# Kernel tuning notes

Measured on AMD Instinct MI355X. Metric: run time of the kernel, lower is better.

The kernel has to match this reference:

```python
import jax, jax.numpy as jnp
import numpy as np

N_NODES = 8192
EMBED = 64
HID = [256, 256, 128]
ACTION = 8192


def setup_inputs() -> dict:
    key = jax.random.key(0)
    ks = jax.random.split(key, 16)
    state = jax.random.uniform(ks[0], (N_NODES, N_NODES), dtype=jnp.float32)
    start = 100  # python int node index
    def u(k, shape, fan_out):
        s = 1.0 / np.sqrt(fan_out)
        return jax.random.uniform(k, shape, minval=-s, maxval=s, dtype=jnp.float32)
    def xav(k, shape):
        s = np.sqrt(6.0 / (shape[0] + shape[1]))
        return jax.random.uniform(k, shape, minval=-s, maxval=s, dtype=jnp.float32)
    in_size = N_NODES + EMBED
    return {
        "state": state,
        "start": start,
        "gc1_w": u(ks[1], (1, HID[0]), HID[0]),
        "gc1_b": u(ks[2], (HID[0],), HID[0]),
        "gc2_w": u(ks[3], (HID[0], EMBED), EMBED),
        "gc2_b": u(ks[4], (EMBED,), EMBED),
        "fc1_w": xav(ks[5], (HID[0], in_size)),
        "fc1_b": jnp.zeros((HID[0],), jnp.float32),
        "fc2_w": xav(ks[6], (HID[1], HID[0])),
        "fc2_b": jnp.zeros((HID[1],), jnp.float32),
        "fc3_w": xav(ks[7], (HID[2], HID[1])),
        "fc3_b": jnp.zeros((HID[2],), jnp.float32),
        "fc4_w": xav(ks[8], (ACTION, HID[2])),
        "fc4_b": jnp.zeros((ACTION,), jnp.float32),
    }


def reference(state, start, gc1_w, gc1_b, gc2_w, gc2_b,
              fc1_w, fc1_b, fc2_w, fc2_b, fc3_w, fc3_b, fc4_w, fc4_b):
    n = state.shape[0]
    # node features = diagonal of state, shape [N, 1]
    x = jnp.diagonal(state)[:, None]
    # adjacency: state with zeroed diagonal, detached (no grad to state via adj)
    idx = jnp.arange(n)
    adj = jax.lax.stop_gradient(state.at[idx, idx].set(0.0))
    # GCN layer 1: spmm(adj, x @ W) + b, relu  (dropout inactive: eval mode)
    h = jax.nn.relu(adj @ (x @ gc1_w) + gc1_b)          # [N, 256]
    # GCN layer 2
    h = jax.nn.relu(adj @ (h @ gc2_w) + gc2_b)          # [N, 64]
    h = jax.nn.log_softmax(h, axis=1)
    start_embedding = h[start]                           # [64]
    start_features = state[start, :]                     # [N]
    e = jnp.concatenate([start_features, start_embedding], axis=-1)  # [N+64]
    y = jax.nn.relu(e @ fc1_w.T + fc1_b)
    y = jax.nn.relu(y @ fc2_w.T + fc2_b)
    y = jax.nn.relu(y @ fc3_w.T + fc3_b)
    end_q = jax.nn.relu(y @ fc4_w.T + fc4_b)             # [action_size]
    return end_q
```

## Files before the change

### kernel.cpp

```cpp
#include <hip/hip_runtime.h>

#define NODES 8192
#define H1 256
#define EMB 64
#define IN_SIZE (NODES + EMB)
#define HID3 128
#define NPART 256

#define X_OFF    0
#define S_OFF    (X_OFF + NODES)
#define PART_OFF (S_OFF + NODES)
#define LS_OFF   (PART_OFF + NPART*H1)
#define Y1_OFF   (LS_OFF + EMB)
#define Y3_OFF   (Y1_OFF + H1)

__device__ __forceinline__ float waveReduceSum(float v) {
    #pragma unroll
    for (int off = 32; off > 0; off >>= 1) v += __shfl_down(v, off, 64);
    return v;
}

__global__ __launch_bounds__(256) void k_diag(const float* __restrict__ state,
                                              float* __restrict__ x) {
    int i = blockIdx.x * 256 + threadIdx.x;
    x[i] = state[(size_t)i * NODES + i];
}

__global__ __launch_bounds__(256) void k_row(const float* __restrict__ state,
                                             const float* __restrict__ x,
                                             float* __restrict__ s) {
    __shared__ float red[4];
    const int i = blockIdx.x;
    const int tid = threadIdx.x;
    const float4* row4 = (const float4*)(state + (size_t)i * NODES);
    const float4* x4   = (const float4*)x;

    float acc = 0.f;
    #pragma unroll
    for (int it = 0; it < NODES / 4 / 256; ++it) {
        int j = tid + it * 256;
        float4 r = row4[j];
        float4 xv = x4[j];
        acc += r.x * xv.x + r.y * xv.y + r.z * xv.z + r.w * xv.w;
    }
    acc = waveReduceSum(acc);
    if ((tid & 63) == 0) red[tid >> 6] = acc;
    __syncthreads();
    if (tid == 0) {
        float xi = x[i];
        s[i] = red[0] + red[1] + red[2] + red[3] - xi * xi;
    }
}

__global__ __launch_bounds__(256) void k_tpart(const float* __restrict__ s,
                                               const float* __restrict__ state,
                                               const int* __restrict__ pstart,
                                               const float* __restrict__ w1,
                                               const float* __restrict__ b1,
                                               float* __restrict__ part) {
    __shared__ float ls_s[32], ls_a[32];
    const int b = blockIdx.x, t = threadIdx.x;
    const int start = *pstart;
    if (t < 32) {
        int i = b * 32 + t;
        ls_s[t] = s[i];
        float a = state[(size_t)start * NODES + i];
        ls_a[t] = (i == start) ? 0.f : a;
    }
    __syncthreads();
    const float w = w1[t], bb = b1[t];
    float acc = 0.f;
    #pragma unroll
    for (int q = 0; q < 32; ++q)
        acc += ls_a[q] * fmaxf(ls_s[q] * w + bb, 0.f);
    part[b * H1 + t] = acc;
}

__global__ __launch_bounds__(256) void k_sm(const float* __restrict__ part,
                                            const float* __restrict__ w2,
                                            const float* __restrict__ b2,
                                            float* __restrict__ ls) {
    __shared__ float ts[H1];
    const int t = threadIdx.x;
    float acc = 0.f;
    #pragma unroll 8
    for (int b = 0; b < NPART; ++b) acc += part[b * H1 + t];
    ts[t] = acc;
    __syncthreads();
    if (t < EMB) {
        float u = 0.f;
        #pragma unroll 8
        for (int j = 0; j < H1; ++j) u += ts[j] * w2[j * EMB + t];
        u = fmaxf(u + b2[t], 0.f);
        float mx = u;
        #pragma unroll
        for (int off = 32; off; off >>= 1) mx = fmaxf(mx, __shfl_xor(mx, off, 64));
        float e = expf(u - mx);
        float se = e;
        #pragma unroll
        for (int off = 32; off; off >>= 1) se += __shfl_xor(se, off, 64);
        ls[t] = (u - mx) - logf(se);
    }
}

__global__ __launch_bounds__(256) void k_fc1(const float* __restrict__ state,
                                             const int* __restrict__ pstart,
                                             const float* __restrict__ ls,
                                             const float* __restrict__ w,
                                             const float* __restrict__ b,
                                             float* __restrict__ y1) {
    __shared__ float red[4];
    const int o = blockIdx.x;
    const int t = threadIdx.x;
    const int start = *pstart;
    const float4* e4 = (const float4*)(state + (size_t)start * NODES);
    const float4* w4 = (const float4*)(w + (size_t)o * IN_SIZE);
    float acc = 0.f;
    #pragma unroll
    for (int it = 0; it < 8; ++it) {
        int j = t + it * 256;
        float4 a = e4[j], ww = w4[j];
        acc += a.x * ww.x + a.y * ww.y + a.z * ww.z + a.w * ww.w;
    }
    if (t < 64) acc += ls[t] * w[(size_t)o * IN_SIZE + NODES + t];
    acc = waveReduceSum(acc);
    if ((t & 63) == 0) red[t >> 6] = acc;
    __syncthreads();
    if (t == 0) y1[o] = fmaxf(red[0] + red[1] + red[2] + red[3] + b[o], 0.f);
}

__global__ __launch_bounds__(256) void k_fc23(const float* __restrict__ y1,
                                              const float* __restrict__ w2_,
                                              const float* __restrict__ b2_,
                                              const float* __restrict__ w3_,
                                              const float* __restrict__ b3_,
                                              float* __restrict__ y3) {
    __shared__ float ly[H1];
    __shared__ float ly2[H1];
    const int t = threadIdx.x;
    ly[t] = y1[t];
    __syncthreads();
    const float4* w4 = (const float4*)(w2_ + (size_t)t * H1);
    float acc = 0.f;
    #pragma unroll
    for (int j = 0; j < 64; ++j) {
        float4 ww = w4[j];
        acc += ww.x * ly[j*4] + ww.y * ly[j*4+1] + ww.z * ly[j*4+2] + ww.w * ly[j*4+3];
    }
    ly2[t] = fmaxf(acc + b2_[t], 0.f);
    __syncthreads();
    if (t < HID3) {
        const float4* w43 = (const float4*)(w3_ + (size_t)t * H1);
        float a3 = 0.f;
        #pragma unroll
        for (int j = 0; j < 64; ++j) {
            float4 ww = w43[j];
            a3 += ww.x * ly2[j*4] + ww.y * ly2[j*4+1] + ww.z * ly2[j*4+2] + ww.w * ly2[j*4+3];
        }
        y3[t] = fmaxf(a3 + b3_[t], 0.f);
    }
}

__global__ __launch_bounds__(256) void k_fc4(const float* __restrict__ y3,
                                             const float* __restrict__ w,
                                             const float* __restrict__ b,
                                             float* __restrict__ out) {
    __shared__ float ly[HID3];
    const int t = threadIdx.x;
    if (t < HID3) ly[t] = y3[t];
    __syncthreads();
    const int wave = t >> 6, lane = t & 63;
    const int o = blockIdx.x * 4 + wave;
    const float* wr = w + (size_t)o * HID3;
    float acc = wr[lane] * ly[lane] + wr[64 + lane] * ly[64 + lane];
    acc = waveReduceSum(acc);
    if (lane == 0) out[o] = fmaxf(acc + b[o], 0.f);
}

extern "C" void kernel_launch(void* const* d_in, const int* in_sizes, int n_in,
                              void* d_out, int out_size, void* d_ws, size_t ws_size,
                              hipStream_t stream) {
    const float* state = (const float*)d_in[0];
    const int*   pstart= (const int*)  d_in[1];
    const float* gc1_w = (const float*)d_in[2];
    const float* gc1_b = (const float*)d_in[3];
    const float* gc2_w = (const float*)d_in[4];
    const float* gc2_b = (const float*)d_in[5];
    const float* fc1_w = (const float*)d_in[6];
    const float* fc1_b = (const float*)d_in[7];
    const float* fc2_w = (const float*)d_in[8];
    const float* fc2_b = (const float*)d_in[9];
    const float* fc3_w = (const float*)d_in[10];
    const float* fc3_b = (const float*)d_in[11];
    const float* fc4_w = (const float*)d_in[12];
    const float* fc4_b = (const float*)d_in[13];
    float* ws = (float*)d_ws;
    float* x    = ws + X_OFF;
    float* s    = ws + S_OFF;
    float* part = ws + PART_OFF;
    float* ls   = ws + LS_OFF;
    float* y1   = ws + Y1_OFF;
    float* y3   = ws + Y3_OFF;
    float* out  = (float*)d_out;

    k_diag <<<NODES / 256, 256, 0, stream>>>(state, x);
    k_row  <<<NODES,       256, 0, stream>>>(state, x, s);
    k_tpart<<<NPART,       256, 0, stream>>>(s, state, pstart, gc1_w, gc1_b, part);
    k_sm   <<<1,           256, 0, stream>>>(part, gc2_w, gc2_b, ls);
    k_fc1  <<<H1,          256, 0, stream>>>(state, pstart, ls, fc1_w, fc1_b, y1);
    k_fc23 <<<1,           256, 0, stream>>>(y1, fc2_w, fc2_b, fc3_w, fc3_b, y3);
    k_fc4  <<<8192 / 4,    256, 0, stream>>>(y3, fc4_w, fc4_b, out);
}
```

Before: 435.4 us.

## Fuse GCN reduction and fc2/fc3 into predecessors via last-block atomics

Merges the partial-sum GCN kernel with the single-block softmax kernel, and the fc1 kernel with the fc2/fc3 kernel. Each pair uses a threadfence plus an atomic counter so the last block to finish does the tail work, which removes two kernel launches and their gaps. The row-dot kernel now handles two rows per block, halving the grid and reusing each x load. The counters are zeroed by the diag kernel, and correctness depends on the fences making the partial results visible to the last block.

```diff
diff --git a/kernel.cpp b/kernel.cpp
--- a/kernel.cpp
+++ b/kernel.cpp
@@ -13,6 +13,7 @@
 #define LS_OFF   (PART_OFF + NPART*H1)
 #define Y1_OFF   (LS_OFF + EMB)
 #define Y3_OFF   (Y1_OFF + H1)
+#define CNT_OFF  (Y3_OFF + HID3)
 
 __device__ __forceinline__ float waveReduceSum(float v) {
     #pragma unroll
@@ -21,44 +22,55 @@
 }
 
 __global__ __launch_bounds__(256) void k_diag(const float* __restrict__ state,
-                                              float* __restrict__ x) {
+                                              float* __restrict__ x,
+                                              int* __restrict__ cnt) {
     int i = blockIdx.x * 256 + threadIdx.x;
     x[i] = state[(size_t)i * NODES + i];
+    if (blockIdx.x == 0 && threadIdx.x < 2) cnt[threadIdx.x] = 0;
 }
 
 __global__ __launch_bounds__(256) void k_row(const float* __restrict__ state,
                                              const float* __restrict__ x,
                                              float* __restrict__ s) {
-    __shared__ float red[4];
-    const int i = blockIdx.x;
+    __shared__ float red[2][4];
+    const int i0 = blockIdx.x * 2;
     const int tid = threadIdx.x;
-    const float4* row4 = (const float4*)(state + (size_t)i * NODES);
-    const float4* x4   = (const float4*)x;
-
-    float acc = 0.f;
+    const float4* r0 = (const float4*)(state + (size_t)i0 * NODES);
+    const float4* r1 = (const float4*)(state + (size_t)(i0 + 1) * NODES);
+    const float4* x4 = (const float4*)x;
+
+    float a0 = 0.f, a1 = 0.f;
     #pragma unroll
     for (int it = 0; it < NODES / 4 / 256; ++it) {
         int j = tid + it * 256;
-        float4 r = row4[j];
         float4 xv = x4[j];
-        acc += r.x * xv.x + r.y * xv.y + r.z * xv.z + r.w * xv.w;
-    }
-    acc = waveReduceSum(acc);
-    if ((tid & 63) == 0) red[tid >> 6] = acc;
-    __syncthreads();
-    if (tid == 0) {
-        float xi = x[i];
-        s[i] = red[0] + red[1] + red[2] + red[3] - xi * xi;
-    }
-}
-
-__global__ __launch_bounds__(256) void k_tpart(const float* __restrict__ s,
-                                               const float* __restrict__ state,
-                                               const int* __restrict__ pstart,
-                                               const float* __restrict__ w1,
-                                               const float* __restrict__ b1,
-                                               float* __restrict__ part) {
+        float4 v0 = r0[j];
+        float4 v1 = r1[j];
+        a0 += v0.x * xv.x + v0.y * xv.y + v0.z * xv.z + v0.w * xv.w;
+        a1 += v1.x * xv.x + v1.y * xv.y + v1.z * xv.z + v1.w * xv.w;
+    }
+    a0 = waveReduceSum(a0);
+    a1 = waveReduceSum(a1);
+    if ((tid & 63) == 0) { red[0][tid >> 6] = a0; red[1][tid >> 6] = a1; }
+    __syncthreads();
+    if (tid < 2) {
+        float xi = x[i0 + tid];
+        s[i0 + tid] = red[tid][0] + red[tid][1] + red[tid][2] + red[tid][3] - xi * xi;
+    }
+}
+
+__global__ __launch_bounds__(256) void k_gcn2(const float* __restrict__ s,
+                                              const float* __restrict__ state,
+                                              const int* __restrict__ pstart,
+                                              const float* __restrict__ w1,
+                                              const float* __restrict__ b1,
+                                              const float* __restrict__ w2,
+                                              const float* __restrict__ b2,
+                                              float* __restrict__ part,
+                                              float* __restrict__ ls,
+                                              int* __restrict__ cnt) {
     __shared__ float ls_s[32], ls_a[32];
+    __shared__ int lastFlag;
     const int b = blockIdx.x, t = threadIdx.x;
     const int start = *pstart;
     if (t < 32) {
@@ -74,18 +86,18 @@
     for (int q = 0; q < 32; ++q)
         acc += ls_a[q] * fmaxf(ls_s[q] * w + bb, 0.f);
     part[b * H1 + t] = acc;
-}
-
-__global__ __launch_bounds__(256) void k_sm(const float* __restrict__ part,
-                                            const float* __restrict__ w2,
-                                            const float* __restrict__ b2,
-                                            float* __restrict__ ls) {
+
+    __threadfence();
+    if (t == 0) lastFlag = (atomicAdd(&cnt[0], 1) == NPART - 1);
+    __syncthreads();
+    if (!lastFlag) return;
+    __threadfence();
+
     __shared__ float ts[H1];
-    const int t = threadIdx.x;
-    float acc = 0.f;
+    float tacc = 0.f;
     #pragma unroll 8
-    for (int b = 0; b < NPART; ++b) acc += part[b * H1 + t];
-    ts[t] = acc;
+    for (int bb2 = 0; bb2 < NPART; ++bb2) tacc += part[bb2 * H1 + t];
+    ts[t] = tacc;
     __syncthreads();
     if (t < EMB) {
         float u = 0.f;
@@ -103,13 +115,20 @@
     }
 }
 
-__global__ __launch_bounds__(256) void k_fc1(const float* __restrict__ state,
-                                             const int* __restrict__ pstart,
-                                             const float* __restrict__ ls,
-                                             const float* __restrict__ w,
-                                             const float* __restrict__ b,
-                                             float* __restrict__ y1) {
+__global__ __launch_bounds__(256) void k_head(const float* __restrict__ state,
+                                              const int* __restrict__ pstart,
+                                              const float* __restrict__ ls,
+                                              const float* __restrict__ w,
+                                              const float* __restrict__ b,
+                                              const float* __restrict__ w2_,
+                                              const float* __restrict__ b2_,
+                                              const float* __restrict__ w3_,
+                                              const float* __restrict__ b3_,
+                                              float* __restrict__ y1,
+                                              float* __restrict__ y3,
+                                              int* __restrict__ cnt) {
     __shared__ float red[4];
+    __shared__ int lastFlag;
     const int o = blockIdx.x;
     const int t = threadIdx.x;
     const int start = *pstart;
@@ -127,34 +146,34 @@
     if ((t & 63) == 0) red[t >> 6] = acc;
     __syncthreads();
     if (t == 0) y1[o] = fmaxf(red[0] + red[1] + red[2] + red[3] + b[o], 0.f);
-}
-
-__global__ __launch_bounds__(256) void k_fc23(const float* __restrict__ y1,
-                                              const float* __restrict__ w2_,
-                                              const float* __restrict__ b2_,
-                                              const float* __restrict__ w3_,
-                                              const float* __restrict__ b3_,
-                                              float* __restrict__ y3) {
+
+    __threadfence();
+    if (t == 0) lastFlag = (atomicAdd(&cnt[1], 1) == H1 - 1);
+    __syncthreads();
+    if (!lastFlag) return;
+    __threadfence();
+
     __shared__ float ly[H1];
     __shared__ float ly2[H1];
-    const int t = threadIdx.x;
     ly[t] = y1[t];
     __syncthreads();
-    const float4* w4 = (const float4*)(w2_ + (size_t)t * H1);
-    float acc = 0.f;
-    #pragma unroll
-    for (int j = 0; j < 64; ++j) {
-        float4 ww = w4[j];
-        acc += ww.x * ly[j*4] + ww.y * ly[j*4+1] + ww.z * ly[j*4+2] + ww.w * ly[j*4+3];
-    }
-    ly2[t] = fmaxf(acc + b2_[t], 0.f);
+    {
+        const float4* wv = (const float4*)(w2_ + (size_t)t * H1);
+        float a2 = 0.f;
+        #pragma unroll
+        for (int j = 0; j < 64; ++j) {
+            float4 ww = wv[j];
+            a2 += ww.x * ly[j*4] + ww.y * ly[j*4+1] + ww.z * ly[j*4+2] + ww.w * ly[j*4+3];
+        }
+        ly2[t] = fmaxf(a2 + b2_[t], 0.f);
+    }
     __syncthreads();
     if (t < HID3) {
-        const float4* w43 = (const float4*)(w3_ + (size_t)t * H1);
+        const float4* wv = (const float4*)(w3_ + (size_t)t * H1);
         float a3 = 0.f;
         #pragma unroll
         for (int j = 0; j < 64; ++j) {
-            float4 ww = w43[j];
+            float4 ww = wv[j];
             a3 += ww.x * ly2[j*4] + ww.y * ly2[j*4+1] + ww.z * ly2[j*4+2] + ww.w * ly2[j*4+3];
         }
         y3[t] = fmaxf(a3 + b3_[t], 0.f);
@@ -201,13 +220,14 @@
     float* ls   = ws + LS_OFF;
     float* y1   = ws + Y1_OFF;
     float* y3   = ws + Y3_OFF;
+    int*   cnt  = (int*)(ws + CNT_OFF);
     float* out  = (float*)d_out;
 
-    k_diag <<<NODES / 256, 256, 0, stream>>>(state, x);
-    k_row  <<<NODES,       256, 0, stream>>>(state, x, s);
-    k_tpart<<<NPART,       256, 0, stream>>>(s, state, pstart, gc1_w, gc1_b, part);
-    k_sm   <<<1,           256, 0, stream>>>(part, gc2_w, gc2_b, ls);
-    k_fc1  <<<H1,          256, 0, stream>>>(state, pstart, ls, fc1_w, fc1_b, y1);
-    k_fc23 <<<1,           256, 0, stream>>>(y1, fc2_w, fc2_b, fc3_w, fc3_b, y3);
-    k_fc4  <<<8192 / 4,    256, 0, stream>>>(y3, fc4_w, fc4_b, out);
-}
+    k_diag <<<NODES / 256, 256, 0, stream>>>(state, x, cnt);
+    k_row  <<<NODES / 2,   256, 0, stream>>>(state, x, s);
+    k_gcn2 <<<NPART,       256, 0, stream>>>(s, state, pstart, gc1_w, gc1_b,
+                                             gc2_w, gc2_b, part, ls, cnt);
+    k_head <<<H1,          256, 0, stream>>>(state, pstart, ls, fc1_w, fc1_b,
+                                             fc2_w, fc2_b, fc3_w, fc3_b, y1, y3, cnt);
+    k_fc4  <<<NODES / 4,   256, 0, stream>>>(y3, fc4_w, fc4_b, out);
+}
```

New measurement: 468.9 us. 1.08x slower.
